# Optimization experiments

Measured on AMD Instinct MI355X. Metric: run time of the kernel, lower is better.

Reference implementation:

```python
import jax, jax.numpy as jnp
import numpy as np

B, S, D = 16, 4096, 64
SCALE = float(np.sqrt(D))  # sqrt(hidden_size)


def setup_inputs() -> dict:
    key = jax.random.key(0)
    kq, kk, kv = jax.random.split(key, 3)
    return {
        "query": jax.random.normal(kq, (B, S, D), dtype=jnp.float32),
        "key": jax.random.normal(kk, (B, S, D), dtype=jnp.float32),
        "value": jax.random.normal(kv, (B, S, D), dtype=jnp.float32),
    }


def reference(query, key, value):
    # energy: [B, S, S]
    energy = jnp.einsum("bqd,bkd->bqk", query, key) / SCALE
    attention = jax.nn.softmax(energy, axis=2)
    return jnp.einsum("bqk,bkd->bqd", attention, value)
```

## Files before the change

kernel.cpp:

```cpp
#include <hip/hip_runtime.h>


#define NBATCH 16
#define SEQ    4096
#define DIM    64
#define BQ     256
#define BK     64
#define NKT    (SEQ / BK)
#define KHALF  (NKT / 2)
#define OELEMS (NBATCH * SEQ * DIM)
#define NROWS  (NBATCH * SEQ)
#define NTILES (NBATCH * NKT)
#define TILEH  4096

#define QSCALE 0.180336879f

typedef _Float16 half2_t __attribute__((ext_vector_type(2)));
typedef _Float16 half4_t __attribute__((ext_vector_type(4)));
typedef _Float16 half8_t __attribute__((ext_vector_type(8)));
typedef float    floatx4 __attribute__((ext_vector_type(4)));

__device__ inline float fast_exp2(float x) {
#if __has_builtin(__builtin_amdgcn_exp2f)
  return __builtin_amdgcn_exp2f(x);
#else
  return exp2f(x);
#endif
}
__device__ inline float fast_rcp(float x) {
#if __has_builtin(__builtin_amdgcn_rcpf)
  return __builtin_amdgcn_rcpf(x);
#else
  return 1.0f / x;
#endif
}

__device__ inline int swz(int row, int col) {
  return row * 64 + ((((col >> 3) ^ ((row >> 1) & 7)) << 3) | (col & 7));
}

__device__ inline void async16(const void* g, void* l) {
  __builtin_amdgcn_global_load_lds(
      (const __attribute__((address_space(1))) void*)g,
      (__attribute__((address_space(3))) void*)l, 16, 0, 0);
}

__global__ __launch_bounds__(256, 2)
void prepack_kv(const float* __restrict__ Kg, const float* __restrict__ Vg,
                _Float16* __restrict__ Kh, _Float16* __restrict__ Vh)
{
  __shared__ __align__(16) _Float16 sKi[TILEH];
  __shared__ __align__(16) _Float16 sVi[TILEH];
  const int tid = threadIdx.x;
  const int t16 = tid & 15;
  const int kg  = tid >> 4;
  const int bt  = blockIdx.x;
  const float* Kt_ = Kg + (size_t)bt * BK * DIM;
  const float* Vt_ = Vg + (size_t)bt * BK * DIM;

  floatx4 kbuf[4], vbuf[4];
  #pragma unroll
  for (int i = 0; i < 4; ++i) {
    const int key = kg + 16 * i;
    kbuf[i] = *(const floatx4*)(Kt_ + key * DIM + t16 * 4);
    vbuf[i] = *(const floatx4*)(Vt_ + key * DIM + t16 * 4);
  }
  #pragma unroll
  for (int i = 0; i < 4; ++i) {
    const int key = kg + 16 * i;
    half4_t h;
    #pragma unroll
    for (int j = 0; j < 4; ++j) h[j] = (_Float16)kbuf[i][j];
    *(half4_t*)&sKi[swz(key, t16 * 4)] = h;
  }
  {
    const int vbase = (kg >> 2) * 8 + (kg & 3) * 2;
    #pragma unroll
    for (int e = 0; e < 4; ++e) {
      const int dim = t16 * 4 + e;
      half2_t h0; h0[0] = (_Float16)vbuf[0][e]; h0[1] = (_Float16)vbuf[1][e];
      half2_t h1; h1[0] = (_Float16)vbuf[2][e]; h1[1] = (_Float16)vbuf[3][e];
      *(half2_t*)&sVi[swz(dim, vbase)]      = h0;
      *(half2_t*)&sVi[swz(dim, vbase + 32)] = h1;
    }
  }
  __syncthreads();
  half8_t* Ko = (half8_t*)(Kh + (size_t)bt * TILEH);
  half8_t* Vo = (half8_t*)(Vh + (size_t)bt * TILEH);
  const half8_t* Ks = (const half8_t*)sKi;
  const half8_t* Vs = (const half8_t*)sVi;
  Ko[tid] = Ks[tid]; Ko[tid + 256] = Ks[tid + 256];
  Vo[tid] = Vs[tid]; Vo[tid + 256] = Vs[tid + 256];
}

__global__ __launch_bounds__(256, 2)
void attn_f16_flash(const float* __restrict__ Qg, const _Float16* __restrict__ Kh,
                    const _Float16* __restrict__ Vh, float* __restrict__ O0g,
                    float* __restrict__ O1g, float* __restrict__ lsg)
{
  __shared__ __align__(16) _Float16 sT[2][2 * TILEH];

  const int tid  = threadIdx.x;
  const int wave = tid >> 6;
  const int lane = tid & 63;
  const int l16  = lane & 15;
  const int quad = lane >> 4;
  const int hK   = (l16 >> 1) & 7;

  const int bid  = blockIdx.x;
  const int half = bid & 1;
  const int qb   = bid >> 1;
  const int b    = qb >> 4;
  const int qt   = qb & 15;
  const int q0   = qt * BQ + wave * 64;
  const int kt0  = half * KHALF;

  const float* Qb = Qg + ((size_t)b * SEQ + q0) * DIM;
  float*       Ob = (half ? O1g : O0g) + ((size_t)b * SEQ + q0) * DIM;
  float*       Ls = lsg + (size_t)half * NROWS + b * SEQ + q0;

  half8_t qf[4][2];
  #pragma unroll
  for (int s = 0; s < 4; ++s)
    #pragma unroll
    for (int c = 0; c < 2; ++c) {
      const floatx4 f0 = *(const floatx4*)(Qb + (s * 16 + l16) * DIM + c * 32 + quad * 8);
      const floatx4 f1 = *(const floatx4*)(Qb + (s * 16 + l16) * DIM + c * 32 + quad * 8 + 4);
      half8_t h;
      #pragma unroll
      for (int j = 0; j < 4; ++j) h[j] = (_Float16)(f0[j] * QSCALE);
      #pragma unroll
      for (int j = 0; j < 4; ++j) h[4 + j] = (_Float16)(f1[j] * QSCALE);
      qf[s][c] = h;
    }

  floatx4 oacc2[4][4];
  float   lsum2[4];
  #pragma unroll
  for (int n = 0; n < 4; ++n)
    #pragma unroll
    for (int s = 0; s < 4; ++s) oacc2[n][s] = (floatx4){0.f, 0.f, 0.f, 0.f};
  #pragma unroll
  for (int s = 0; s < 4; ++s) lsum2[s] = 0.f;

  #define ASYNC(KT, BUF)                                                       \
    do {                                                                       \
      const char* gk = (const char*)(Kh + ((size_t)b * NKT + (KT)) * TILEH)    \
                       + wave * 2048;                                          \
      const char* gv = (const char*)(Vh + ((size_t)b * NKT + (KT)) * TILEH)    \
                       + wave * 2048;                                          \
      char* lk = (char*)(&sT[BUF][0])     + wave * 2048;                       \
      char* lv = (char*)(&sT[BUF][TILEH]) + wave * 2048;                       \
      async16(gk + lane * 16,        lk);                                      \
      async16(gk + 1024 + lane * 16, lk + 1024);                               \
      async16(gv + lane * 16,        lv);                                      \
      async16(gv + 1024 + lane * 16, lv + 1024);                               \
    } while (0)

  #define COMPUTE(BUF)                                                         \
    do {                                                                       \
      const _Float16* SKB = &sT[BUF][0];                                       \
      const _Float16* SVB = &sT[BUF][TILEH];                                   \
      _Pragma("unroll")                                                        \
      for (int h = 0; h < 2; ++h) {                                            \
        floatx4 sc2[2][4];                                                     \
        _Pragma("unroll")                                                      \
        for (int k2 = 0; k2 < 2; ++k2)                                         \
          _Pragma("unroll")                                                    \
          for (int s = 0; s < 4; ++s) sc2[k2][s] = (floatx4){0.f, 0.f, 0.f, 0.f};\
        _Pragma("unroll")                                                      \
        for (int k2 = 0; k2 < 2; ++k2) {                                       \
          const int nk = h * 2 + k2;                                           \
          _Pragma("unroll")                                                    \
          for (int c = 0; c < 2; ++c) {                                        \
            half8_t kf = *(const half8_t*)&SKB[(nk * 16 + l16) * 64 +          \
                                               (((c * 4 + quad) ^ hK) << 3)];  \
            _Pragma("unroll")                                                  \
            for (int s = 0; s < 4; ++s)                                        \
              sc2[k2][s] = __builtin_amdgcn_mfma_f32_16x16x32_f16(             \
                  kf, qf[s][c], sc2[k2][s], 0, 0, 0);                          \
          }                                                                    \
        }                                                                      \
        half8_t bfr[4];                                                        \
        _Pragma("unroll")                                                      \
        for (int s = 0; s < 4; ++s) {                                          \
          half8_t bf;                                                          \
          _Pragma("unroll")                                                    \
          for (int j = 0; j < 8; ++j) {                                        \
            float p = fast_exp2(sc2[j & 1][s][j >> 1]);                        \
            lsum2[s] += p;                                                     \
            bf[j] = (_Float16)p;                                               \
          }                                                                    \
          bfr[s] = bf;                                                         \
        }                                                                      \
        _Pragma("unroll")                                                      \
        for (int n = 0; n < 4; ++n) {                                          \
          half8_t vf = *(const half8_t*)&SVB[(n * 16 + l16) * 64 +             \
                                             (((h * 4 + quad) ^ hK) << 3)];    \
          _Pragma("unroll")                                                    \
          for (int s = 0; s < 4; ++s)                                          \
            oacc2[n][s] = __builtin_amdgcn_mfma_f32_16x16x32_f16(              \
                vf, bfr[s], oacc2[n][s], 0, 0, 0);                             \
        }                                                                      \
      }                                                                        \
    } while (0)

  ASYNC(kt0, 0);
  __syncthreads();

  #pragma unroll 1
  for (int t = 0; t < (KHALF - 2) / 2; ++t) {
    ASYNC(kt0 + 2 * t + 1, 1);
    COMPUTE(0);
    __syncthreads();
    ASYNC(kt0 + 2 * t + 2, 0);
    COMPUTE(1);
    __syncthreads();
  }
  ASYNC(kt0 + KHALF - 1, 1);
  COMPUTE(0);
  __syncthreads();
  COMPUTE(1);

  #pragma unroll
  for (int s = 0; s < 4; ++s) {
    float v = lsum2[s];
    v += __shfl_xor(v, 16);
    v += __shfl_xor(v, 32);
    if (lane < 16) Ls[s * 16 + l16] = v;
  }
  #pragma unroll
  for (int s = 0; s < 4; ++s)
    #pragma unroll
    for (int n = 0; n < 4; ++n)
      *(floatx4*)&Ob[(s * 16 + l16) * DIM + n * 16 + quad * 4] = oacc2[n][s];

  #undef ASYNC
  #undef COMPUTE
}

__global__ __launch_bounds__(256)
void attn_combine(float* __restrict__ O, const float* __restrict__ O1,
                  const float* __restrict__ lsg)
{
  const int i = blockIdx.x * 256 + threadIdx.x;
  const int row = i >> 4;
  const float inv = fast_rcp(lsg[row] + lsg[NROWS + row]);
  const float4 a  = ((const float4*)O)[i];
  const float4 bb = ((const float4*)O1)[i];
  float4 r;
  r.x = (a.x + bb.x) * inv;
  r.y = (a.y + bb.y) * inv;
  r.z = (a.z + bb.z) * inv;
  r.w = (a.w + bb.w) * inv;
  ((float4*)O)[i] = r;
}

extern "C" void kernel_launch(void* const* d_in, const int* in_sizes, int n_in,
                              void* d_out, int out_size, void* d_ws, size_t ws_size,
                              hipStream_t stream) {
  const float* Q = (const float*)d_in[0];
  const float* K = (const float*)d_in[1];
  const float* V = (const float*)d_in[2];
  float* O  = (float*)d_out;
  (void)in_sizes; (void)n_in; (void)out_size; (void)ws_size;

  float*     O1 = (float*)d_ws;
  float*     Ls = O1 + OELEMS;
  _Float16*  Kh = (_Float16*)(Ls + 2 * NROWS);
  _Float16*  Vh = Kh + (size_t)NTILES * TILEH;

  prepack_kv<<<dim3(NTILES), dim3(256), 0, stream>>>(K, V, Kh, Vh);
  attn_f16_flash<<<dim3(2 * NBATCH * (SEQ / BQ)), dim3(256), 0, stream>>>(
      Q, Kh, Vh, O, O1, Ls);
  attn_combine<<<dim3(OELEMS / 4 / 256), dim3(256), 0, stream>>>(O, O1, Ls);
}
```

Baseline: 167.5 us.

## Split key range four ways and store partial outputs in fp16

Raises the split-K factor from two to four, so the flash kernel launches 1024 blocks instead of 512, which fills the GPU's compute units better. Splits 1-3 write their unnormalized partial outputs as fp16 to cut workspace traffic, and the combine kernel sums four partials and four row sums. The trade-off is more partial-output traffic and combine work, plus extra prologue and epilogue overhead per block. Storing partials in fp16 also costs some accuracy.

```diff
diff --git a/kernel.cpp b/kernel.cpp
--- a/kernel.cpp
+++ b/kernel.cpp
@@ -7,7 +7,8 @@
 #define BQ     256
 #define BK     64
 #define NKT    (SEQ / BK)
-#define KHALF  (NKT / 2)
+#define NSPLIT 4
+#define KQ     (NKT / NSPLIT)
 #define OELEMS (NBATCH * SEQ * DIM)
 #define NROWS  (NBATCH * SEQ)
 #define NTILES (NBATCH * NKT)
@@ -96,7 +97,7 @@
 __global__ __launch_bounds__(256, 2)
 void attn_f16_flash(const float* __restrict__ Qg, const _Float16* __restrict__ Kh,
                     const _Float16* __restrict__ Vh, float* __restrict__ O0g,
-                    float* __restrict__ O1g, float* __restrict__ lsg)
+                    _Float16* __restrict__ Pg, float* __restrict__ lsg)
 {
   __shared__ __align__(16) _Float16 sT[2][2 * TILEH];
 
@@ -107,17 +108,16 @@
   const int quad = lane >> 4;
   const int hK   = (l16 >> 1) & 7;
 
-  const int bid  = blockIdx.x;
-  const int half = bid & 1;
-  const int qb   = bid >> 1;
-  const int b    = qb >> 4;
-  const int qt   = qb & 15;
-  const int q0   = qt * BQ + wave * 64;
-  const int kt0  = half * KHALF;
+  const int bid   = blockIdx.x;
+  const int split = bid & (NSPLIT - 1);
+  const int qb    = bid >> 2;
+  const int b     = qb >> 4;
+  const int qt    = qb & 15;
+  const int q0    = qt * BQ + wave * 64;
+  const int kt0   = split * KQ;
 
   const float* Qb = Qg + ((size_t)b * SEQ + q0) * DIM;
-  float*       Ob = (half ? O1g : O0g) + ((size_t)b * SEQ + q0) * DIM;
-  float*       Ls = lsg + (size_t)half * NROWS + b * SEQ + q0;
+  float*       Ls = lsg + (size_t)split * NROWS + b * SEQ + q0;
 
   half8_t qf[4][2];
   #pragma unroll
@@ -209,7 +209,7 @@
   __syncthreads();
 
   #pragma unroll 1
-  for (int t = 0; t < (KHALF - 2) / 2; ++t) {
+  for (int t = 0; t < (KQ - 2) / 2; ++t) {
     ASYNC(kt0 + 2 * t + 1, 1);
     COMPUTE(0);
     __syncthreads();
@@ -217,7 +217,7 @@
     COMPUTE(1);
     __syncthreads();
   }
-  ASYNC(kt0 + KHALF - 1, 1);
+  ASYNC(kt0 + KQ - 1, 1);
   COMPUTE(0);
   __syncthreads();
   COMPUTE(1);
@@ -229,30 +229,49 @@
     v += __shfl_xor(v, 32);
     if (lane < 16) Ls[s * 16 + l16] = v;
   }
-  #pragma unroll
-  for (int s = 0; s < 4; ++s)
-    #pragma unroll
-    for (int n = 0; n < 4; ++n)
-      *(floatx4*)&Ob[(s * 16 + l16) * DIM + n * 16 + quad * 4] = oacc2[n][s];
+  const size_t obase = ((size_t)b * SEQ + q0) * DIM;
+  if (split == 0) {
+    float* Ob = O0g + obase;
+    #pragma unroll
+    for (int s = 0; s < 4; ++s)
+      #pragma unroll
+      for (int n = 0; n < 4; ++n)
+        *(floatx4*)&Ob[(s * 16 + l16) * DIM + n * 16 + quad * 4] = oacc2[n][s];
+  } else {
+    _Float16* Ob = Pg + (size_t)(split - 1) * OELEMS + obase;
+    #pragma unroll
+    for (int s = 0; s < 4; ++s)
+      #pragma unroll
+      for (int n = 0; n < 4; ++n) {
+        const floatx4 v = oacc2[n][s];
+        half4_t h;
+        #pragma unroll
+        for (int j = 0; j < 4; ++j) h[j] = (_Float16)v[j];
+        *(half4_t*)&Ob[(s * 16 + l16) * DIM + n * 16 + quad * 4] = h;
+      }
+  }
 
   #undef ASYNC
   #undef COMPUTE
 }
 
 __global__ __launch_bounds__(256)
-void attn_combine(float* __restrict__ O, const float* __restrict__ O1,
+void attn_combine(float* __restrict__ O, const _Float16* __restrict__ Pg,
                   const float* __restrict__ lsg)
 {
   const int i = blockIdx.x * 256 + threadIdx.x;
   const int row = i >> 4;
-  const float inv = fast_rcp(lsg[row] + lsg[NROWS + row]);
-  const float4 a  = ((const float4*)O)[i];
-  const float4 bb = ((const float4*)O1)[i];
+  const float inv = fast_rcp(lsg[row] + lsg[NROWS + row] +
+                             lsg[2 * NROWS + row] + lsg[3 * NROWS + row]);
+  const float4  a  = ((const float4*)O)[i];
+  const half4_t p1 = ((const half4_t*)Pg)[i];
+  const half4_t p2 = ((const half4_t*)(Pg + (size_t)OELEMS))[i];
+  const half4_t p3 = ((const half4_t*)(Pg + 2 * (size_t)OELEMS))[i];
   float4 r;
-  r.x = (a.x + bb.x) * inv;
-  r.y = (a.y + bb.y) * inv;
-  r.z = (a.z + bb.z) * inv;
-  r.w = (a.w + bb.w) * inv;
+  r.x = (a.x + (float)p1[0] + (float)p2[0] + (float)p3[0]) * inv;
+  r.y = (a.y + (float)p1[1] + (float)p2[1] + (float)p3[1]) * inv;
+  r.z = (a.z + (float)p1[2] + (float)p2[2] + (float)p3[2]) * inv;
+  r.w = (a.w + (float)p1[3] + (float)p2[3] + (float)p3[3]) * inv;
   ((float4*)O)[i] = r;
 }
 
@@ -265,13 +284,13 @@
   float* O  = (float*)d_out;
   (void)in_sizes; (void)n_in; (void)out_size; (void)ws_size;
 
-  float*     O1 = (float*)d_ws;
-  float*     Ls = O1 + OELEMS;
-  _Float16*  Kh = (_Float16*)(Ls + 2 * NROWS);
-  _Float16*  Vh = Kh + (size_t)NTILES * TILEH;
+  _Float16* P  = (_Float16*)d_ws;
+  float*    Ls = (float*)(P + 3 * (size_t)OELEMS);
+  _Float16* Kh = (_Float16*)(Ls + 4 * (size_t)NROWS);
+  _Float16* Vh = Kh + (size_t)NTILES * TILEH;
 
   prepack_kv<<<dim3(NTILES), dim3(256), 0, stream>>>(K, V, Kh, Vh);
-  attn_f16_flash<<<dim3(2 * NBATCH * (SEQ / BQ)), dim3(256), 0, stream>>>(
-      Q, Kh, Vh, O, O1, Ls);
-  attn_combine<<<dim3(OELEMS / 4 / 256), dim3(256), 0, stream>>>(O, O1, Ls);
-}
+  attn_f16_flash<<<dim3(NSPLIT * NBATCH * (SEQ / BQ)), dim3(256), 0, stream>>>(
+      Q, Kh, Vh, O, P, Ls);
+  attn_combine<<<dim3(OELEMS / 4 / 256), dim3(256), 0, stream>>>(O, P, Ls);
+}
```

Measured after the change: 174.4 us. +4.1%, slower.

## Load K/V fragments directly from global memory instead of staging in LDS

Applied to the files above, without the earlier changes.

Removes the double-buffered LDS staging (async global-to-LDS loads and block barriers), so each wave reads its K and V MFMA fragments straight from global memory with an unswizzled packed layout. It also remaps block indices so that consecutive blocks cover different batches, which changes L2 locality, and it raises wave priority around the MFMA sections with s_setprio. The aim is to drop the barrier and LDS overhead and rely on L2/cache reuse across the four waves. The cost is that each wave now issues its own global loads of the same tiles, with no explicit prefetch to hide their latency.

```diff
diff --git a/kernel.cpp b/kernel.cpp
--- a/kernel.cpp
+++ b/kernel.cpp
@@ -35,15 +35,7 @@
 #endif
 }
 
-__device__ inline int swz(int row, int col) {
-  return row * 64 + ((((col >> 3) ^ ((row >> 1) & 7)) << 3) | (col & 7));
-}
-
-__device__ inline void async16(const void* g, void* l) {
-  __builtin_amdgcn_global_load_lds(
-      (const __attribute__((address_space(1))) void*)g,
-      (__attribute__((address_space(3))) void*)l, 16, 0, 0);
-}
+__device__ inline int swz(int row, int col) { return row * 64 + col; }
 
 __global__ __launch_bounds__(256, 2)
 void prepack_kv(const float* __restrict__ Kg, const float* __restrict__ Vg,
@@ -98,20 +90,18 @@
                     const _Float16* __restrict__ Vh, float* __restrict__ O0g,
                     float* __restrict__ O1g, float* __restrict__ lsg)
 {
-  __shared__ __align__(16) _Float16 sT[2][2 * TILEH];
-
   const int tid  = threadIdx.x;
   const int wave = tid >> 6;
   const int lane = tid & 63;
   const int l16  = lane & 15;
   const int quad = lane >> 4;
-  const int hK   = (l16 >> 1) & 7;
 
   const int bid  = blockIdx.x;
-  const int half = bid & 1;
-  const int qb   = bid >> 1;
-  const int b    = qb >> 4;
-  const int qt   = qb & 15;
+  const int x    = bid & 7;
+  const int r    = bid >> 3;
+  const int b    = x + ((r & 1) << 3);
+  const int qt   = (r >> 1) & 15;
+  const int half = (r >> 5) & 1;
   const int q0   = qt * BQ + wave * 64;
   const int kt0  = half * KHALF;
 
@@ -143,84 +133,60 @@
   #pragma unroll
   for (int s = 0; s < 4; ++s) lsum2[s] = 0.f;
 
-  #define ASYNC(KT, BUF)                                                       \
-    do {                                                                       \
-      const char* gk = (const char*)(Kh + ((size_t)b * NKT + (KT)) * TILEH)    \
-                       + wave * 2048;                                          \
-      const char* gv = (const char*)(Vh + ((size_t)b * NKT + (KT)) * TILEH)    \
-                       + wave * 2048;                                          \
-      char* lk = (char*)(&sT[BUF][0])     + wave * 2048;                       \
-      char* lv = (char*)(&sT[BUF][TILEH]) + wave * 2048;                       \
-      async16(gk + lane * 16,        lk);                                      \
-      async16(gk + 1024 + lane * 16, lk + 1024);                               \
-      async16(gv + lane * 16,        lv);                                      \
-      async16(gv + 1024 + lane * 16, lv + 1024);                               \
-    } while (0)
-
-  #define COMPUTE(BUF)                                                         \
-    do {                                                                       \
-      const _Float16* SKB = &sT[BUF][0];                                       \
-      const _Float16* SVB = &sT[BUF][TILEH];                                   \
-      _Pragma("unroll")                                                        \
-      for (int h = 0; h < 2; ++h) {                                            \
-        floatx4 sc2[2][4];                                                     \
-        _Pragma("unroll")                                                      \
-        for (int k2 = 0; k2 < 2; ++k2)                                         \
-          _Pragma("unroll")                                                    \
-          for (int s = 0; s < 4; ++s) sc2[k2][s] = (floatx4){0.f, 0.f, 0.f, 0.f};\
-        _Pragma("unroll")                                                      \
-        for (int k2 = 0; k2 < 2; ++k2) {                                       \
-          const int nk = h * 2 + k2;                                           \
-          _Pragma("unroll")                                                    \
-          for (int c = 0; c < 2; ++c) {                                        \
-            half8_t kf = *(const half8_t*)&SKB[(nk * 16 + l16) * 64 +          \
-                                               (((c * 4 + quad) ^ hK) << 3)];  \
-            _Pragma("unroll")                                                  \
-            for (int s = 0; s < 4; ++s)                                        \
-              sc2[k2][s] = __builtin_amdgcn_mfma_f32_16x16x32_f16(             \
-                  kf, qf[s][c], sc2[k2][s], 0, 0, 0);                          \
-          }                                                                    \
-        }                                                                      \
-        half8_t bfr[4];                                                        \
-        _Pragma("unroll")                                                      \
-        for (int s = 0; s < 4; ++s) {                                          \
-          half8_t bf;                                                          \
-          _Pragma("unroll")                                                    \
-          for (int j = 0; j < 8; ++j) {                                        \
-            float p = fast_exp2(sc2[j & 1][s][j >> 1]);                        \
-            lsum2[s] += p;                                                     \
-            bf[j] = (_Float16)p;                                               \
-          }                                                                    \
-          bfr[s] = bf;                                                         \
-        }                                                                      \
-        _Pragma("unroll")                                                      \
-        for (int n = 0; n < 4; ++n) {                                          \
-          half8_t vf = *(const half8_t*)&SVB[(n * 16 + l16) * 64 +             \
-                                             (((h * 4 + quad) ^ hK) << 3)];    \
-          _Pragma("unroll")                                                    \
-          for (int s = 0; s < 4; ++s)                                          \
-            oacc2[n][s] = __builtin_amdgcn_mfma_f32_16x16x32_f16(              \
-                vf, bfr[s], oacc2[n][s], 0, 0, 0);                             \
-        }                                                                      \
-      }                                                                        \
-    } while (0)
-
-  ASYNC(kt0, 0);
-  __syncthreads();
+  const _Float16* Kb = Kh + ((size_t)b * NKT + kt0) * TILEH;
+  const _Float16* Vb = Vh + ((size_t)b * NKT + kt0) * TILEH;
 
   #pragma unroll 1
-  for (int t = 0; t < (KHALF - 2) / 2; ++t) {
-    ASYNC(kt0 + 2 * t + 1, 1);
-    COMPUTE(0);
-    __syncthreads();
-    ASYNC(kt0 + 2 * t + 2, 0);
-    COMPUTE(1);
-    __syncthreads();
-  }
-  ASYNC(kt0 + KHALF - 1, 1);
-  COMPUTE(0);
-  __syncthreads();
-  COMPUTE(1);
+  for (int t = 0; t < KHALF; ++t) {
+    const _Float16* KT = Kb + (size_t)t * TILEH;
+    const _Float16* VT = Vb + (size_t)t * TILEH;
+    #pragma unroll
+    for (int h = 0; h < 2; ++h) {
+      floatx4 sc2[2][4];
+      #pragma unroll
+      for (int k2 = 0; k2 < 2; ++k2)
+        #pragma unroll
+        for (int s = 0; s < 4; ++s) sc2[k2][s] = (floatx4){0.f, 0.f, 0.f, 0.f};
+      __builtin_amdgcn_s_setprio(1);
+      #pragma unroll
+      for (int k2 = 0; k2 < 2; ++k2) {
+        const int nk = h * 2 + k2;
+        #pragma unroll
+        for (int c = 0; c < 2; ++c) {
+          const half8_t kf = *(const half8_t*)&KT[(nk * 16 + l16) * 64 +
+                                                  ((c * 4 + quad) << 3)];
+          #pragma unroll
+          for (int s = 0; s < 4; ++s)
+            sc2[k2][s] = __builtin_amdgcn_mfma_f32_16x16x32_f16(
+                kf, qf[s][c], sc2[k2][s], 0, 0, 0);
+        }
+      }
+      __builtin_amdgcn_s_setprio(0);
+      half8_t bfr[4];
+      #pragma unroll
+      for (int s = 0; s < 4; ++s) {
+        half8_t bf;
+        #pragma unroll
+        for (int j = 0; j < 8; ++j) {
+          float p = fast_exp2(sc2[j & 1][s][j >> 1]);
+          lsum2[s] += p;
+          bf[j] = (_Float16)p;
+        }
+        bfr[s] = bf;
+      }
+      __builtin_amdgcn_s_setprio(1);
+      #pragma unroll
+      for (int n = 0; n < 4; ++n) {
+        const half8_t vf = *(const half8_t*)&VT[(n * 16 + l16) * 64 +
+                                                ((h * 4 + quad) << 3)];
+        #pragma unroll
+        for (int s = 0; s < 4; ++s)
+          oacc2[n][s] = __builtin_amdgcn_mfma_f32_16x16x32_f16(
+              vf, bfr[s], oacc2[n][s], 0, 0, 0);
+      }
+      __builtin_amdgcn_s_setprio(0);
+    }
+  }
 
   #pragma unroll
   for (int s = 0; s < 4; ++s) {
@@ -234,9 +200,6 @@
     #pragma unroll
     for (int n = 0; n < 4; ++n)
       *(floatx4*)&Ob[(s * 16 + l16) * DIM + n * 16 + quad * 4] = oacc2[n][s];
-
-  #undef ASYNC
-  #undef COMPUTE
 }
 
 __global__ __launch_bounds__(256)
```

Result: slower. 221.1 us (+32.0%).

## Deepen K/V async pipeline to four LDS buffers with vmcnt gating

Applied to the files above, without the earlier changes.

Expands the shared-memory staging from two to four K/V tile buffers, prefetches two tiles ahead, and replaces full __syncthreads with an explicit vmcnt wait plus a single barrier per tile. It also raises wave priority around the MFMA blocks and remaps block indices so consecutive blocks cover different batches and the two key halves are farther apart. The goal is to hide global-load latency behind more compute and to spread blocks across L2 more evenly. In exchange, the doubled LDS use (64KB per block) may cut occupancy below the two blocks per CU the launch bounds request. The dynamic buffer index t&3 also risks register or addressing overhead.

```diff
diff --git a/kernel.cpp b/kernel.cpp
--- a/kernel.cpp
+++ b/kernel.cpp
@@ -98,7 +98,7 @@
                     const _Float16* __restrict__ Vh, float* __restrict__ O0g,
                     float* __restrict__ O1g, float* __restrict__ lsg)
 {
-  __shared__ __align__(16) _Float16 sT[2][2 * TILEH];
+  __shared__ __align__(16) _Float16 sT[4][2 * TILEH];
 
   const int tid  = threadIdx.x;
   const int wave = tid >> 6;
@@ -108,10 +108,11 @@
   const int hK   = (l16 >> 1) & 7;
 
   const int bid  = blockIdx.x;
-  const int half = bid & 1;
-  const int qb   = bid >> 1;
-  const int b    = qb >> 4;
-  const int qt   = qb & 15;
+  const int x    = bid & 7;
+  const int r    = bid >> 3;
+  const int b    = x + ((r & 1) << 3);
+  const int qt   = (r >> 1) & 15;
+  const int half = (r >> 5) & 1;
   const int q0   = qt * BQ + wave * 64;
   const int kt0  = half * KHALF;
 
@@ -168,6 +169,7 @@
         for (int k2 = 0; k2 < 2; ++k2)                                         \
           _Pragma("unroll")                                                    \
           for (int s = 0; s < 4; ++s) sc2[k2][s] = (floatx4){0.f, 0.f, 0.f, 0.f};\
+        __builtin_amdgcn_s_setprio(1);                                         \
         _Pragma("unroll")                                                      \
         for (int k2 = 0; k2 < 2; ++k2) {                                       \
           const int nk = h * 2 + k2;                                           \
@@ -181,6 +183,7 @@
                   kf, qf[s][c], sc2[k2][s], 0, 0, 0);                          \
           }                                                                    \
         }                                                                      \
+        __builtin_amdgcn_s_setprio(0);                                         \
         half8_t bfr[4];                                                        \
         _Pragma("unroll")                                                      \
         for (int s = 0; s < 4; ++s) {                                          \
@@ -193,6 +196,7 @@
           }                                                                    \
           bfr[s] = bf;                                                         \
         }                                                                      \
+        __builtin_amdgcn_s_setprio(1);                                         \
         _Pragma("unroll")                                                      \
         for (int n = 0; n < 4; ++n) {                                          \
           half8_t vf = *(const half8_t*)&SVB[(n * 16 + l16) * 64 +             \
@@ -202,25 +206,30 @@
             oacc2[n][s] = __builtin_amdgcn_mfma_f32_16x16x32_f16(              \
                 vf, bfr[s], oacc2[n][s], 0, 0, 0);                             \
         }                                                                      \
+        __builtin_amdgcn_s_setprio(0);                                         \
       }                                                                        \
     } while (0)
 
-  ASYNC(kt0, 0);
-  __syncthreads();
+  #define GATE(N)                                                              \
+    do {                                                                       \
+      asm volatile("s_waitcnt vmcnt(" #N ")" ::: "memory");                    \
+      __builtin_amdgcn_s_barrier();                                            \
+      __builtin_amdgcn_sched_barrier(0);                                       \
+    } while (0)
+
+  ASYNC(kt0 + 0, 0);
+  ASYNC(kt0 + 1, 1);
 
   #pragma unroll 1
-  for (int t = 0; t < (KHALF - 2) / 2; ++t) {
-    ASYNC(kt0 + 2 * t + 1, 1);
-    COMPUTE(0);
-    __syncthreads();
-    ASYNC(kt0 + 2 * t + 2, 0);
-    COMPUTE(1);
-    __syncthreads();
-  }
-  ASYNC(kt0 + KHALF - 1, 1);
-  COMPUTE(0);
-  __syncthreads();
-  COMPUTE(1);
+  for (int t = 0; t < KHALF - 2; ++t) {
+    GATE(4);
+    ASYNC(kt0 + t + 2, (t + 2) & 3);
+    COMPUTE(t & 3);
+  }
+  GATE(4);
+  COMPUTE((KHALF - 2) & 3);
+  GATE(0);
+  COMPUTE((KHALF - 1) & 3);
 
   #pragma unroll
   for (int s = 0; s < 4; ++s) {
@@ -237,6 +246,7 @@
 
   #undef ASYNC
   #undef COMPUTE
+  #undef GATE
 }
 
 __global__ __launch_bounds__(256)
```

Result: faster. 163.6 us (-2.3%).
